# Performance work log

Hardware: AMD Instinct MI355X
Metric: run time of the kernel (lower is better)

The kernel has to match this reference:

```python
import jax, jax.numpy as jnp
import numpy as np
import math

D_MODEL = 2048
N_HEADS = 16
D_K = D_MODEL // N_HEADS
B = 4
S = 2048


def setup_inputs() -> dict:
    key = jax.random.key(0)
    ks = jax.random.split(key, 12)
    sd = 1.0 / math.sqrt(D_MODEL)
    inp = {
        "query": jax.random.normal(ks[0], (B, S, D_MODEL), dtype=jnp.float32),
        "key": jax.random.normal(ks[1], (B, S, D_MODEL), dtype=jnp.float32),
        "value": jax.random.normal(ks[2], (B, S, D_MODEL), dtype=jnp.float32),
        # causal mask: 1 where attendable, 0 where masked (mask == 0 -> -1e9)
        "mask": jnp.tril(jnp.ones((1, 1, S, S), dtype=jnp.int32)),
        "W_q": jax.random.uniform(ks[3], (D_MODEL, D_MODEL), jnp.float32, -sd, sd),
        "b_q": jnp.zeros((D_MODEL,), jnp.float32),
        "W_k": jax.random.uniform(ks[4], (D_MODEL, D_MODEL), jnp.float32, -sd, sd),
        "b_k": jnp.zeros((D_MODEL,), jnp.float32),
        "W_v": jax.random.uniform(ks[5], (D_MODEL, D_MODEL), jnp.float32, -sd, sd),
        "b_v": jnp.zeros((D_MODEL,), jnp.float32),
        "W_o": jax.random.uniform(ks[6], (D_MODEL, D_MODEL), jnp.float32, -sd, sd),
        "b_o": jnp.zeros((D_MODEL,), jnp.float32),
    }
    return inp


def reference(query, key, value, mask, W_q, b_q, W_k, b_k, W_v, b_v, W_o, b_o):
    scale = math.sqrt(D_K)
    # QKV projections + split heads: [B, S, D] -> [B, H, S, d_k]
    def split_heads(x):
        return x.reshape(B, -1, N_HEADS, D_K).transpose(0, 2, 1, 3)

    Q = split_heads(query @ W_q.T + b_q)
    K = split_heads(key @ W_k.T + b_k)
    V = split_heads(value @ W_v.T + b_v)

    # scores: [B, H, Sq, Sk]
    scores = jnp.einsum("bhqd,bhkd->bhqk", Q, K) / scale
    scores = jnp.where(mask == 0, jnp.float32(-1e9), scores)
    attn = jax.nn.softmax(scores, axis=-1)
    # context: [B, H, Sq, d_k] -> [B, Sq, D]
    ctx = jnp.einsum("bhqk,bhkd->bhqd", attn, V)
    ctx = ctx.transpose(0, 2, 1, 3).reshape(B, S, D_MODEL)
    return ctx @ W_o.T + b_o
```

## Files before the change

kernel.cpp:

```cpp
#include <hip/hip_runtime.h>
#include <stdint.h>

#define D_MODEL 2048
#define S_LEN 2048
#define BATCH 4
#define NHEADS 16
#define DK 128
#define M_TOK (BATCH * S_LEN)

typedef __attribute__((ext_vector_type(8))) short bf16x8;
typedef __attribute__((ext_vector_type(4))) float f32x4;

__device__ __forceinline__ short f2bf(float f) {
  unsigned u = __float_as_uint(f);
  u = (u + 0x7FFF + ((u >> 16) & 1)) >> 16;
  return (short)u;
}

__device__ __forceinline__ void gl2lds16(const void* g, void* l) {
  __builtin_amdgcn_global_load_lds(
      (const __attribute__((address_space(1))) unsigned int*)g,
      (__attribute__((address_space(3))) unsigned int*)l, 16, 0, 0);
}

#define ASM_BAR() asm volatile("s_barrier" ::: "memory")
#define VMCNT0() asm volatile("s_waitcnt vmcnt(0)" ::: "memory")

__global__ __launch_bounds__(256) void cvt_kernel(const float* __restrict__ in,
                                                  short* __restrict__ out,
                                                  int n8) {
  int i = blockIdx.x * blockDim.x + threadIdx.x;
  const int stride = gridDim.x * blockDim.x;
  for (; i < n8; i += stride) {
    const float4* p = (const float4*)(in + (size_t)i * 8);
    float4 a = p[0], b = p[1];
    bf16x8 o;
    o[0] = f2bf(a.x); o[1] = f2bf(a.y); o[2] = f2bf(a.z); o[3] = f2bf(a.w);
    o[4] = f2bf(b.x); o[5] = f2bf(b.y); o[6] = f2bf(b.z); o[7] = f2bf(b.w);
    *(bf16x8*)(out + (size_t)i * 8) = o;
  }
}

template <int EPI>
__global__ __launch_bounds__(512, 2) void gemm256(const short* __restrict__ A,
                                                  const short* __restrict__ B,
                                                  const float* __restrict__ bias,
                                                  void* __restrict__ Cout) {
  __shared__ short As[2][256 * 64];
  __shared__ short Bs[2][256 * 64];
  const int t = threadIdx.x, lane = t & 63, w = t >> 6;
  const int c = lane & 15, g = lane >> 4;
  const int wr = w >> 2, wc = w & 3;

  const int cpx = (int)gridDim.x >> 3;
  const int swz = ((int)blockIdx.x & 7) * cpx + ((int)blockIdx.x >> 3);
  const int by = swz >> 3, bx = swz & 7;
  const int row0 = by * 256, col0 = bx * 256;
  const int K = D_MODEL;
  const int NT = K / 64;

  const int srow = t >> 3;
  const int sseg = t & 7;
  const int skk = 8 * (sseg ^ (srow & 7));

  const short* Abase = A + (size_t)(row0 + srow) * K;
  const short* Bbase = B + (size_t)(col0 + srow) * K;

#define SWEEPA(p, R, kt)                                              \
  gl2lds16(Abase + (size_t)(R) * 64 * K + (kt) * 64 + skk,            \
           &As[p][(R) * 4096 + t * 8])
#define SWEEPB(p, R, kt)                                              \
  gl2lds16(Bbase + (size_t)(R) * 64 * K + (kt) * 64 + skk,            \
           &Bs[p][(R) * 4096 + t * 8])
#define STAGE_TILE(q, kt1)                                            \
  {                                                                   \
    SWEEPA(q, 0, kt1); SWEEPA(q, 1, kt1);                             \
    SWEEPA(q, 2, kt1); SWEEPA(q, 3, kt1);                             \
    SWEEPB(q, 0, kt1); SWEEPB(q, 1, kt1);                             \
    SWEEPB(q, 2, kt1); SWEEPB(q, 3, kt1);                             \
  }

  f32x4 acc[8][4] = {};

  STAGE_TILE(0, 0);

  for (int kt = 0; kt < NT; ++kt) {
    const int p = kt & 1, q = p ^ 1;
    VMCNT0();
    ASM_BAR();
    if (kt + 1 < NT) STAGE_TILE(q, kt + 1);

    const char* abase = (const char*)As[p];
    const char* bbase = (const char*)Bs[p];
#pragma unroll
    for (int ks = 0; ks < 2; ++ks) {
      const int kb = (ks * 64 + g * 16) ^ ((c & 7) << 4);
      bf16x8 bfr[4];
#pragma unroll
      for (int ni = 0; ni < 4; ++ni)
        bfr[ni] = *(const bf16x8*)(bbase + (wc * 64 + ni * 16 + c) * 128 + kb);
#pragma unroll
      for (int mg = 0; mg < 2; ++mg) {
        bf16x8 afr[4];
#pragma unroll
        for (int mi = 0; mi < 4; ++mi)
          afr[mi] = *(const bf16x8*)(abase +
                                     (wr * 128 + mg * 64 + mi * 16 + c) * 128 +
                                     kb);
        __builtin_amdgcn_s_setprio(1);
#pragma unroll
        for (int mi = 0; mi < 4; ++mi)
#pragma unroll
          for (int ni = 0; ni < 4; ++ni)
            acc[mg * 4 + mi][ni] = __builtin_amdgcn_mfma_f32_16x16x32_bf16(
                afr[mi], bfr[ni], acc[mg * 4 + mi][ni], 0, 0, 0);
        __builtin_amdgcn_s_setprio(0);
      }
    }
  }

#pragma unroll
  for (int ni = 0; ni < 4; ++ni) {
    const int col = col0 + wc * 64 + ni * 16 + c;
    const float bv = bias[col];
#pragma unroll
    for (int m = 0; m < 8; ++m) {
      const int rbase = row0 + wr * 128 + (m >> 2) * 64 + (m & 3) * 16 + g * 4;
      if (EPI == 2) {
        const int h = col >> 7, dk = col & 127;
        const int b = rbase >> 11, s0 = rbase & 2047;
        ushort4 pk;
        pk.x = (unsigned short)f2bf(acc[m][ni][0] + bv);
        pk.y = (unsigned short)f2bf(acc[m][ni][1] + bv);
        pk.z = (unsigned short)f2bf(acc[m][ni][2] + bv);
        pk.w = (unsigned short)f2bf(acc[m][ni][3] + bv);
        *(ushort4*)&((short*)Cout)[(((size_t)b * NHEADS + h) * DK + dk) *
                                       S_LEN + s0] = pk;
      } else {
#pragma unroll
        for (int r = 0; r < 4; ++r) {
          const int row = rbase + r;
          const float v = acc[m][ni][r] + bv;
          if (EPI == 0) {
            const int b = row >> 11, s = row & 2047;
            const int h = col >> 7, dk = col & 127;
            ((short*)Cout)[(((size_t)b * NHEADS + h) * S_LEN + s) * DK + dk] =
                f2bf(v);
          } else {
            ((float*)Cout)[(size_t)row * D_MODEL + col] = v;
          }
        }
      }
    }
  }
#undef SWEEPA
#undef SWEEPB
#undef STAGE_TILE
}

__global__ __launch_bounds__(256, 2) void attn_kernel(
    const short* __restrict__ Qp, const short* __restrict__ Kp,
    const short* __restrict__ Vt, short* __restrict__ ctx) {
  const int t = threadIdx.x, lane = t & 63, w = t >> 6;
  const int c = lane & 15, g = lane >> 4;

  const int fid = blockIdx.x;
  const int x = fid & 7, u = fid >> 3;
  const int bh = ((u & 7) << 3) | x;
  const int qt = 15 - (u >> 3);
  const int b = bh >> 4, h = bh & 15;

  __shared__ short Kl[2][64 * 128];
  __shared__ short Vl[2][128 * 64];
  __shared__ short Pl[4][32][64];

  const short* Kbase = Kp + (size_t)bh * S_LEN * DK;
  const short* Vbase = Vt + (size_t)bh * DK * S_LEN;

  const int qbase = qt * 128 + w * 32;
  const short* Qg = Qp + ((size_t)bh * S_LEN + qbase + c) * DK;
  bf16x8 aq[2][4];
#pragma unroll
  for (int mi = 0; mi < 2; ++mi)
#pragma unroll
    for (int kc = 0; kc < 4; ++kc)
      aq[mi][kc] = *(const bf16x8*)(Qg + mi * 16 * DK + kc * 32 + g * 8);

  float mprev[2][4], lsum[2][4];
  f32x4 accO[2][8] = {};
#pragma unroll
  for (int mi = 0; mi < 2; ++mi)
#pragma unroll
    for (int r = 0; r < 4; ++r) {
      mprev[mi][r] = -3.0e38f;
      lsum[mi][r] = 0.f;
    }
  const float cexp = 0.12753101829629947f;

  const int nt = 2 * qt + 2;
  const int jmax = (qbase + 31) >> 6;

  auto stage = [&](int buf, int j) {
    const short* Kg = Kbase + (size_t)j * 64 * DK;
#pragma unroll
    for (int ii = 0; ii < 4; ++ii) {
      int s = t + 256 * ii;
      int row = s >> 4, cs = s & 15;
      gl2lds16(Kg + row * DK + (cs ^ (row & 7)) * 8, &Kl[buf][s * 8]);
    }
    const short* Vg = Vbase + j * 64;
#pragma unroll
    for (int ii = 0; ii < 4; ++ii) {
      int s = t + 256 * ii;
      int row = s >> 3, cs = s & 7;
      gl2lds16(Vg + (size_t)row * S_LEN + (cs ^ (row & 7)) * 8,
               &Vl[buf][s * 8]);
    }
  };

  stage(0, 0);
  __syncthreads();
  int cur = 0;

  for (int j = 0; j < nt; ++j) {
    if (j + 1 < nt) stage(cur ^ 1, j + 1);

    if (j <= jmax) {
      f32x4 sa[2][4];
#pragma unroll
      for (int mi = 0; mi < 2; ++mi)
#pragma unroll
        for (int nf = 0; nf < 4; ++nf) sa[mi][nf] = (f32x4){0.f, 0.f, 0.f, 0.f};
      __builtin_amdgcn_s_setprio(1);
#pragma unroll
      for (int nf = 0; nf < 4; ++nf) {
#pragma unroll
        for (int kc = 0; kc < 4; ++kc) {
          const int row = nf * 16 + c;
          const int seg = kc * 4 + g;
          bf16x8 bk = *(const bf16x8*)((const char*)&Kl[cur][0] + row * 256 +
                                       ((seg ^ (row & 7)) << 4));
#pragma unroll
          for (int mi = 0; mi < 2; ++mi)
            sa[mi][nf] = __builtin_amdgcn_mfma_f32_16x16x32_bf16(
                aq[mi][kc], bk, sa[mi][nf], 0, 0, 0);
        }
      }
      __builtin_amdgcn_s_setprio(0);

#pragma unroll
      for (int mi = 0; mi < 2; ++mi) {
        if (j * 64 + 63 > qbase + mi * 16) {
#pragma unroll
          for (int r = 0; r < 4; ++r) {
            const int qglob = qbase + mi * 16 + g * 4 + r;
#pragma unroll
            for (int nf = 0; nf < 4; ++nf)
              if ((j * 64 + nf * 16 + c) > qglob) sa[mi][nf][r] = -3.0e38f;
          }
        }
      }

      float lmax[2][4];
      bool need = false;
#pragma unroll
      for (int mi = 0; mi < 2; ++mi)
#pragma unroll
        for (int r = 0; r < 4; ++r) {
          const float m0 = fmaxf(fmaxf(sa[mi][0][r], sa[mi][1][r]),
                                 fmaxf(sa[mi][2][r], sa[mi][3][r]));
          lmax[mi][r] = m0;
          need = need || (m0 > mprev[mi][r] + 40.f);
        }
      if (__any((int)need)) {
#pragma unroll
        for (int mi = 0; mi < 2; ++mi)
#pragma unroll
          for (int r = 0; r < 4; ++r) {
            float m0 = lmax[mi][r];
            m0 = fmaxf(m0, __shfl_xor(m0, 1));
            m0 = fmaxf(m0, __shfl_xor(m0, 2));
            m0 = fmaxf(m0, __shfl_xor(m0, 4));
            m0 = fmaxf(m0, __shfl_xor(m0, 8));
            const float nm = fmaxf(mprev[mi][r], m0);
            const float corr = exp2f((mprev[mi][r] - nm) * cexp);
            lsum[mi][r] *= corr;
#pragma unroll
            for (int no = 0; no < 8; ++no) accO[mi][no][r] *= corr;
            mprev[mi][r] = nm;
          }
      }

#pragma unroll
      for (int mi = 0; mi < 2; ++mi)
#pragma unroll
        for (int r = 0; r < 4; ++r) {
          const float nm = mprev[mi][r];
          const int prow = mi * 16 + g * 4 + r;
          float rs = 0.f;
#pragma unroll
          for (int nf = 0; nf < 4; ++nf) {
            const float pp = exp2f((sa[mi][nf][r] - nm) * cexp);
            rs += pp;
            const int col = nf * 16 + c;
            *(short*)((char*)&Pl[w][0][0] + prow * 128 +
                      (((col >> 3) ^ (prow & 7)) << 4) + (col & 7) * 2) =
                f2bf(pp);
          }
          lsum[mi][r] += rs;
        }

      bf16x8 ap[2][2];
#pragma unroll
      for (int mi = 0; mi < 2; ++mi)
#pragma unroll
        for (int kc = 0; kc < 2; ++kc) {
          const int prow = mi * 16 + c;
          const int kseg = kc * 4 + g;
          ap[mi][kc] = *(const bf16x8*)((const char*)&Pl[w][0][0] +
                                        prow * 128 +
                                        ((kseg ^ (prow & 7)) << 4));
        }
      __builtin_amdgcn_s_setprio(1);
#pragma unroll
      for (int no = 0; no < 8; ++no) {
#pragma unroll
        for (int kc = 0; kc < 2; ++kc) {
          const int row = no * 16 + c;
          const int seg = kc * 4 + g;
          bf16x8 bv = *(const bf16x8*)((const char*)&Vl[cur][0] + row * 128 +
                                       ((seg ^ (row & 7)) << 4));
#pragma unroll
          for (int mi = 0; mi < 2; ++mi)
            accO[mi][no] = __builtin_amdgcn_mfma_f32_16x16x32_bf16(
                ap[mi][kc], bv, accO[mi][no], 0, 0, 0);
        }
      }
      __builtin_amdgcn_s_setprio(0);
    }

    __syncthreads();
    cur ^= 1;
  }

#pragma unroll
  for (int mi = 0; mi < 2; ++mi) {
    const int qrow = qbase + mi * 16 + g * 4;
#pragma unroll
    for (int r = 0; r < 4; ++r) {
      float ls = lsum[mi][r];
      ls += __shfl_xor(ls, 1);
      ls += __shfl_xor(ls, 2);
      ls += __shfl_xor(ls, 4);
      ls += __shfl_xor(ls, 8);
      const float inv = 1.f / ls;
#pragma unroll
      for (int no = 0; no < 8; ++no) {
        ctx[((size_t)b * S_LEN + qrow + r) * D_MODEL + h * DK + no * 16 + c] =
            f2bf(accO[mi][no][r] * inv);
      }
    }
  }
}

extern "C" void kernel_launch(void* const* d_in, const int* in_sizes, int n_in,
                              void* d_out, int out_size, void* d_ws,
                              size_t ws_size, hipStream_t stream) {
  const float* query = (const float*)d_in[0];
  const float* key = (const float*)d_in[1];
  const float* value = (const float*)d_in[2];
  const float* W_q = (const float*)d_in[4];
  const float* b_q = (const float*)d_in[5];
  const float* W_k = (const float*)d_in[6];
  const float* b_k = (const float*)d_in[7];
  const float* W_v = (const float*)d_in[8];
  const float* b_v = (const float*)d_in[9];
  const float* W_o = (const float*)d_in[10];
  const float* b_o = (const float*)d_in[11];
  float* out = (float*)d_out;

  char* p = (char*)d_ws;
  const size_t WSZ = (size_t)D_MODEL * D_MODEL * 2;
  const size_t XSZ = (size_t)M_TOK * D_MODEL * 2;
  short* wq = (short*)p; p += WSZ;
  short* wk = (short*)p; p += WSZ;
  short* wv = (short*)p; p += WSZ;
  short* wo = (short*)p; p += WSZ;
  short* xq = (short*)p; p += XSZ;
  short* xk = (short*)p; p += XSZ;
  short* xv = (short*)p; p += XSZ;
  short* Qp = (short*)p; p += XSZ;
  short* Kp = (short*)p; p += XSZ;

  const int nX8 = (M_TOK * D_MODEL) / 8;
  const int nW8 = (D_MODEL * D_MODEL) / 8;
  cvt_kernel<<<2048, 256, 0, stream>>>(query, xq, nX8);
  cvt_kernel<<<2048, 256, 0, stream>>>(key, xk, nX8);
  cvt_kernel<<<2048, 256, 0, stream>>>(value, xv, nX8);
  cvt_kernel<<<2048, 256, 0, stream>>>(W_q, wq, nW8);
  cvt_kernel<<<2048, 256, 0, stream>>>(W_k, wk, nW8);
  cvt_kernel<<<2048, 256, 0, stream>>>(W_v, wv, nW8);
  cvt_kernel<<<2048, 256, 0, stream>>>(W_o, wo, nW8);

  const int ngemm = (M_TOK / 256) * (D_MODEL / 256);
  gemm256<0><<<ngemm, 512, 0, stream>>>(xq, wq, b_q, Qp);
  gemm256<0><<<ngemm, 512, 0, stream>>>(xk, wk, b_k, Kp);
  gemm256<2><<<ngemm, 512, 0, stream>>>(xv, wv, b_v, xk);

  attn_kernel<<<dim3(16 * BATCH * NHEADS), 256, 0, stream>>>(Qp, Kp, xk, xq);

  gemm256<1><<<ngemm, 512, 0, stream>>>(xq, wo, b_o, out);
}
```

Before: 505.2 us.

## Batch conversions and QKV GEMMs into fewer launches, fold softmax scale into Q

Merges the seven fp32->bf16 conversion launches into two (activations and weights) and the three QKV projection GEMMs into one launch with a z-dimension. The softmax log2e/sqrt(dk) factor is folded into the Q projection epilogue, removing a multiply per score in attention, and the rescale threshold is adjusted to match the new units. Attention also uses a cheaper truncating-round bf16 conversion for P and the output. This cuts launch overhead and tail effects, and the larger QKV grid fills the GPU better. In exchange Q is rounded to bf16 after scaling and the fast bf16 rounding ignores ties and NaN handling. V now goes to a separate Vt workspace buffer instead of reusing xk.

```diff
diff --git a/kernel.cpp b/kernel.cpp
--- a/kernel.cpp
+++ b/kernel.cpp
@@ -16,6 +16,9 @@
   u = (u + 0x7FFF + ((u >> 16) & 1)) >> 16;
   return (short)u;
 }
+__device__ __forceinline__ short f2bf_fast(float f) {
+  return (short)((__float_as_uint(f) + 0x8000u) >> 16);
+}
 
 __device__ __forceinline__ void gl2lds16(const void* g, void* l) {
   __builtin_amdgcn_global_load_lds(
@@ -26,9 +29,13 @@
 #define ASM_BAR() asm volatile("s_barrier" ::: "memory")
 #define VMCNT0() asm volatile("s_waitcnt vmcnt(0)" ::: "memory")
 
-__global__ __launch_bounds__(256) void cvt_kernel(const float* __restrict__ in,
-                                                  short* __restrict__ out,
-                                                  int n8) {
+__global__ __launch_bounds__(256) void cvt3_kernel(const float* __restrict__ a0,
+                                                   const float* __restrict__ a1,
+                                                   const float* __restrict__ a2,
+                                                   short* o0, short* o1,
+                                                   short* o2, int n8) {
+  const float* in = (blockIdx.y == 0) ? a0 : (blockIdx.y == 1) ? a1 : a2;
+  short* out = (blockIdx.y == 0) ? o0 : (blockIdx.y == 1) ? o1 : o2;
   int i = blockIdx.x * blockDim.x + threadIdx.x;
   const int stride = gridDim.x * blockDim.x;
   for (; i < n8; i += stride) {
@@ -41,18 +48,46 @@
   }
 }
 
-template <int EPI>
-__global__ __launch_bounds__(512, 2) void gemm256(const short* __restrict__ A,
-                                                  const short* __restrict__ B,
-                                                  const float* __restrict__ bias,
-                                                  void* __restrict__ Cout) {
-  __shared__ short As[2][256 * 64];
-  __shared__ short Bs[2][256 * 64];
+__global__ __launch_bounds__(256) void cvt4_kernel(const float* __restrict__ a0,
+                                                   const float* __restrict__ a1,
+                                                   const float* __restrict__ a2,
+                                                   const float* __restrict__ a3,
+                                                   short* o0, short* o1,
+                                                   short* o2, short* o3,
+                                                   int n8) {
+  const float* in = (blockIdx.y == 0)   ? a0
+                    : (blockIdx.y == 1) ? a1
+                    : (blockIdx.y == 2) ? a2
+                                        : a3;
+  short* out = (blockIdx.y == 0)   ? o0
+               : (blockIdx.y == 1) ? o1
+               : (blockIdx.y == 2) ? o2
+                                   : o3;
+  int i = blockIdx.x * blockDim.x + threadIdx.x;
+  const int stride = gridDim.x * blockDim.x;
+  for (; i < n8; i += stride) {
+    const float4* p = (const float4*)(in + (size_t)i * 8);
+    float4 a = p[0], b = p[1];
+    bf16x8 o;
+    o[0] = f2bf(a.x); o[1] = f2bf(a.y); o[2] = f2bf(a.z); o[3] = f2bf(a.w);
+    o[4] = f2bf(b.x); o[5] = f2bf(b.y); o[6] = f2bf(b.z); o[7] = f2bf(b.w);
+    *(bf16x8*)(out + (size_t)i * 8) = o;
+  }
+}
+
+__device__ __forceinline__ void gemm_body(const short* __restrict__ A,
+                                          const short* __restrict__ B,
+                                          const float* __restrict__ bias,
+                                          void* __restrict__ Cout, int epi,
+                                          float escale, short* AsBase,
+                                          short* BsBase) {
+  short(*As)[256 * 64] = (short(*)[256 * 64])AsBase;
+  short(*Bs)[256 * 64] = (short(*)[256 * 64])BsBase;
   const int t = threadIdx.x, lane = t & 63, w = t >> 6;
   const int c = lane & 15, g = lane >> 4;
   const int wr = w >> 2, wc = w & 3;
 
-  const int cpx = (int)gridDim.x >> 3;
+  const int cpx = 32;
   const int swz = ((int)blockIdx.x & 7) * cpx + ((int)blockIdx.x >> 3);
   const int by = swz >> 3, bx = swz & 7;
   const int row0 = by * 256, col0 = bx * 256;
@@ -126,7 +161,7 @@
 #pragma unroll
     for (int m = 0; m < 8; ++m) {
       const int rbase = row0 + wr * 128 + (m >> 2) * 64 + (m & 3) * 16 + g * 4;
-      if (EPI == 2) {
+      if (epi == 2) {
         const int h = col >> 7, dk = col & 127;
         const int b = rbase >> 11, s0 = rbase & 2047;
         ushort4 pk;
@@ -136,19 +171,21 @@
         pk.w = (unsigned short)f2bf(acc[m][ni][3] + bv);
         *(ushort4*)&((short*)Cout)[(((size_t)b * NHEADS + h) * DK + dk) *
                                        S_LEN + s0] = pk;
-      } else {
+      } else if (epi == 0) {
 #pragma unroll
         for (int r = 0; r < 4; ++r) {
           const int row = rbase + r;
-          const float v = acc[m][ni][r] + bv;
-          if (EPI == 0) {
-            const int b = row >> 11, s = row & 2047;
-            const int h = col >> 7, dk = col & 127;
-            ((short*)Cout)[(((size_t)b * NHEADS + h) * S_LEN + s) * DK + dk] =
-                f2bf(v);
-          } else {
-            ((float*)Cout)[(size_t)row * D_MODEL + col] = v;
-          }
+          const float v = (acc[m][ni][r] + bv) * escale;
+          const int b = row >> 11, s = row & 2047;
+          const int h = col >> 7, dk = col & 127;
+          ((short*)Cout)[(((size_t)b * NHEADS + h) * S_LEN + s) * DK + dk] =
+              f2bf(v);
+        }
+      } else {
+#pragma unroll
+        for (int r = 0; r < 4; ++r) {
+          const int row = rbase + r;
+          ((float*)Cout)[(size_t)row * D_MODEL + col] = acc[m][ni][r] + bv;
         }
       }
     }
@@ -156,6 +193,34 @@
 #undef SWEEPA
 #undef SWEEPB
 #undef STAGE_TILE
+}
+
+__global__ __launch_bounds__(512, 2) void gemm_qkv(
+    const short* __restrict__ xq, const short* __restrict__ xk,
+    const short* __restrict__ xv, const short* __restrict__ wq,
+    const short* __restrict__ wk, const short* __restrict__ wv,
+    const float* __restrict__ bq, const float* __restrict__ bk,
+    const float* __restrict__ bv, short* Qp, short* Kp, short* Vt,
+    float qscale) {
+  __shared__ short As[2][256 * 64];
+  __shared__ short Bs[2][256 * 64];
+  const int z = blockIdx.y;
+  const short* A = (z == 0) ? xq : (z == 1) ? xk : xv;
+  const short* B = (z == 0) ? wq : (z == 1) ? wk : wv;
+  const float* bias = (z == 0) ? bq : (z == 1) ? bk : bv;
+  void* C = (z == 0) ? (void*)Qp : (z == 1) ? (void*)Kp : (void*)Vt;
+  const int epi = (z == 2) ? 2 : 0;
+  const float esc = (z == 0) ? qscale : 1.0f;
+  gemm_body(A, B, bias, C, epi, esc, &As[0][0], &Bs[0][0]);
+}
+
+__global__ __launch_bounds__(512, 2) void gemm_o(const short* __restrict__ A,
+                                                 const short* __restrict__ B,
+                                                 const float* __restrict__ bias,
+                                                 float* Cout) {
+  __shared__ short As[2][256 * 64];
+  __shared__ short Bs[2][256 * 64];
+  gemm_body(A, B, bias, Cout, 1, 1.0f, &As[0][0], &Bs[0][0]);
 }
 
 __global__ __launch_bounds__(256, 2) void attn_kernel(
@@ -195,7 +260,6 @@
       mprev[mi][r] = -3.0e38f;
       lsum[mi][r] = 0.f;
     }
-  const float cexp = 0.12753101829629947f;
 
   const int nt = 2 * qt + 2;
   const int jmax = (qbase + 31) >> 6;
@@ -270,7 +334,7 @@
           const float m0 = fmaxf(fmaxf(sa[mi][0][r], sa[mi][1][r]),
                                  fmaxf(sa[mi][2][r], sa[mi][3][r]));
           lmax[mi][r] = m0;
-          need = need || (m0 > mprev[mi][r] + 40.f);
+          need = need || (m0 > mprev[mi][r] + 5.101f);
         }
       if (__any((int)need)) {
 #pragma unroll
@@ -283,7 +347,7 @@
             m0 = fmaxf(m0, __shfl_xor(m0, 4));
             m0 = fmaxf(m0, __shfl_xor(m0, 8));
             const float nm = fmaxf(mprev[mi][r], m0);
-            const float corr = exp2f((mprev[mi][r] - nm) * cexp);
+            const float corr = exp2f(mprev[mi][r] - nm);
             lsum[mi][r] *= corr;
 #pragma unroll
             for (int no = 0; no < 8; ++no) accO[mi][no][r] *= corr;
@@ -300,12 +364,12 @@
           float rs = 0.f;
 #pragma unroll
           for (int nf = 0; nf < 4; ++nf) {
-            const float pp = exp2f((sa[mi][nf][r] - nm) * cexp);
+            const float pp = exp2f(sa[mi][nf][r] - nm);
             rs += pp;
             const int col = nf * 16 + c;
             *(short*)((char*)&Pl[w][0][0] + prow * 128 +
                       (((col >> 3) ^ (prow & 7)) << 4) + (col & 7) * 2) =
-                f2bf(pp);
+                f2bf_fast(pp);
           }
           lsum[mi][r] += rs;
         }
@@ -357,7 +421,7 @@
 #pragma unroll
       for (int no = 0; no < 8; ++no) {
         ctx[((size_t)b * S_LEN + qrow + r) * D_MODEL + h * DK + no * 16 + c] =
-            f2bf(accO[mi][no][r] * inv);
+            f2bf_fast(accO[mi][no][r] * inv);
       }
     }
   }
@@ -394,20 +458,18 @@
 
   const int nX8 = (M_TOK * D_MODEL) / 8;
   const int nW8 = (D_MODEL * D_MODEL) / 8;
-  cvt_kernel<<<2048, 256, 0, stream>>>(query, xq, nX8);
-  cvt_kernel<<<2048, 256, 0, stream>>>(key, xk, nX8);
-  cvt_kernel<<<2048, 256, 0, stream>>>(value, xv, nX8);
-  cvt_kernel<<<2048, 256, 0, stream>>>(W_q, wq, nW8);
-  cvt_kernel<<<2048, 256, 0, stream>>>(W_k, wk, nW8);
-  cvt_kernel<<<2048, 256, 0, stream>>>(W_v, wv, nW8);
-  cvt_kernel<<<2048, 256, 0, stream>>>(W_o, wo, nW8);
-
-  const int ngemm = (M_TOK / 256) * (D_MODEL / 256);
-  gemm256<0><<<ngemm, 512, 0, stream>>>(xq, wq, b_q, Qp);
-  gemm256<0><<<ngemm, 512, 0, stream>>>(xk, wk, b_k, Kp);
-  gemm256<2><<<ngemm, 512, 0, stream>>>(xv, wv, b_v, xk);
-
-  attn_kernel<<<dim3(16 * BATCH * NHEADS), 256, 0, stream>>>(Qp, Kp, xk, xq);
-
-  gemm256<1><<<ngemm, 512, 0, stream>>>(xq, wo, b_o, out);
-}
+  cvt3_kernel<<<dim3(1024, 3), 256, 0, stream>>>(query, key, value, xq, xk, xv,
+                                                 nX8);
+  cvt4_kernel<<<dim3(512, 4), 256, 0, stream>>>(W_q, W_k, W_v, W_o, wq, wk, wv,
+                                                wo, nW8);
+
+  const float qscale = 0.12753101829629947f;
+  short* Vt = (short*)p;
+
+  gemm_qkv<<<dim3(256, 3), 512, 0, stream>>>(xq, xk, xv, wq, wk, wv, b_q, b_k,
+                                             b_v, Qp, Kp, Vt, qscale);
+
+  attn_kernel<<<dim3(16 * BATCH * NHEADS), 256, 0, stream>>>(Qp, Kp, Vt, xq);
+
+  gemm_o<<<256, 512, 0, stream>>>(xq, wo, b_o, out);
+}
```

After: 508.8 us. Within noise of the previous version (+0.7%).
